# Optimization experiments

Hardware: AMD Instinct MI355X
Metric: run time of the kernel (lower is better)

Reference implementation:

```python
import jax, jax.numpy as jnp
import numpy as np

RADIUS = 0.2
NSAMPLE = 32
BANDWIDTH = 0.1


def ellipsoid_query(xyz, new_xyz, radius, nsample):
    """xyz:(B,N,3), new_xyz:(B,P,3) -> idx:(B,P,nsample) int32.
    Ellipsoid semi-axes (radius, 2*radius, radius); first nsample hits,
    padded with the first hit (index 0 if empty), matching the CUDA kernel.
    """
    B, N, _ = xyz.shape
    inv_sq = jnp.asarray([1.0 / radius**2, 1.0 / (2.0 * radius) ** 2, 1.0 / radius**2],
                         dtype=xyz.dtype)
    # accumulate per-coordinate to avoid a (B,P,N,3) intermediate
    q = jnp.zeros((B, new_xyz.shape[1], N), dtype=xyz.dtype)
    for k in range(3):
        d = new_xyz[:, :, None, k] - xyz[:, None, :, k]  # (B,P,N)
        q = q + d * d * inv_sq[k]
    mask = q < 1.0
    cand = jnp.where(mask, jnp.arange(N, dtype=jnp.int32), jnp.int32(N))  # invalid -> N
    cand = jnp.sort(cand, axis=-1)[..., :nsample]                          # (B,P,S)
    first = cand[..., :1]
    first = jnp.where(first >= N, jnp.int32(0), first)
    return jnp.where(cand >= N, first, cand)


def group(features, idx):
    """features:(B,C,N), idx:(B,P,S) -> (B,C,P,S)"""
    return jnp.take_along_axis(features[:, :, None, :], idx[:, None, :, :], axis=-1)


def setup_inputs() -> dict:
    key = jax.random.key(0)
    k1, k2, k3 = jax.random.split(key, 3)
    xyz = jax.random.uniform(k1, (4, 8192, 3), dtype=jnp.float32)
    new_xyz = jax.random.uniform(k2, (4, 2048, 3), dtype=jnp.float32)
    features = jax.random.normal(k3, (4, 64, 8192), dtype=jnp.float32)
    return {"xyz": xyz, "new_xyz": new_xyz, "features": features}


def reference(xyz, new_xyz, features):
    idx = ellipsoid_query(xyz, new_xyz, RADIUS, NSAMPLE)          # (B,P,S)
    xyz_trans = jnp.transpose(xyz, (0, 2, 1))                      # (B,3,N)
    grouped_xyz = group(xyz_trans, idx)                            # (B,3,P,S)
    # density: gaussian of distance to center
    g = jnp.transpose(grouped_xyz, (0, 2, 3, 1))                   # (B,P,S,3)
    dist = jnp.linalg.norm(g - new_xyz[:, :, None, :], axis=-1)    # (B,P,S)
    density = jnp.exp(-dist**2 / (2.0 * BANDWIDTH**2)) / (2.5 * BANDWIDTH)
    grouped_density = (1.0 / density)[:, None, :, :]               # (B,1,P,S)
    grouped_features = group(features, idx)                        # (B,C,P,S)
    return jnp.concatenate([grouped_xyz, grouped_density, grouped_features], axis=1)
```

## Files before the change

### kernel.cpp

```cpp
#include <hip/hip_runtime.h>

constexpr int NPTS = 8192;
constexpr int NQ   = 2048;
constexpr int NC   = 64;
constexpr int NS   = 32;
constexpr int NCH  = 3 + 1 + NC;
constexpr int CS   = NQ * NS;


__global__ __launch_bounds__(256, 8) void prep_kernel(
    const float* __restrict__ feat,
    const float* __restrict__ xyz,
    float* __restrict__ ftr,
    float* __restrict__ soa)
{
    const int b  = blockIdx.y;
    const int bx = blockIdx.x;
    const int t  = threadIdx.x;

    if (bx < NPTS / 64) {
        __shared__ float tile[NC][65];
        const int n0 = bx * 64;
        const float* fb = feat + (size_t)b * NC * NPTS;
        {
            const int pl = t & 63;
            const int c0 = t >> 6;
            #pragma unroll
            for (int i = 0; i < 16; ++i) {
                const int c = c0 + 4 * i;
                tile[c][pl] = fb[(size_t)c * NPTS + n0 + pl];
            }
        }
        __syncthreads();
        float* tb = ftr + ((size_t)b * NPTS + n0) * NC;
        {
            const int cl = t & 63;
            const int pb = t >> 6;
            #pragma unroll
            for (int i = 0; i < 16; ++i) {
                const int pp = pb + 4 * i;
                tb[(size_t)pp * NC + cl] = tile[cl][pp];
            }
        }
    } else {
        const int n0 = (bx - NPTS / 64) * 4096;
        const float* xb = xyz + (size_t)b * NPTS * 3;
        float* xs = soa + (size_t)b * 3 * NPTS;
        float* ys = xs + NPTS;
        float* zs = ys + NPTS;
        #pragma unroll
        for (int k = 0; k < 16; ++k) {
            const int i = n0 + k * 256 + t;
            xs[i] = xb[i * 3 + 0];
            ys[i] = xb[i * 3 + 1];
            zs[i] = xb[i * 3 + 2];
        }
    }
}

__global__ __launch_bounds__(256, 8) void scan_kernel(
    const float* __restrict__ soa,
    const float* __restrict__ nxyz,
    int* __restrict__ gidx,
    float* __restrict__ out)
{
    __shared__ int idx_s[4][NS];

    const int b    = blockIdx.y;
    const int tid  = threadIdx.x;
    const int lane = tid & 63;
    const int wave = tid >> 6;
    const int p    = blockIdx.x * 4 + wave;

    const float* xs = soa + (size_t)b * 3 * NPTS;
    const float* ys = xs + NPTS;
    const float* zs = ys + NPTS;
    int* idx_row = idx_s[wave];

    const float qx = nxyz[((size_t)b * NQ + p) * 3 + 0];
    const float qy = nxyz[((size_t)b * NQ + p) * 3 + 1];
    const float qz = nxyz[((size_t)b * NQ + p) * 3 + 2];

    int cnt = 0;
    int first = -1;

    float x0 = xs[lane],      y0 = ys[lane],      z0 = zs[lane];
    float x1 = xs[64 + lane], y1 = ys[64 + lane], z1 = zs[64 + lane];

    for (int base = 0; base < NPTS; base += 64) {
        float xn = 0.f, yn = 0.f, zn = 0.f;
        const int pf = base + 128;
        if (pf < NPTS) {
            xn = xs[pf + lane]; yn = ys[pf + lane]; zn = zs[pf + lane];
        }

        const float dx = __fsub_rn(qx, x0);
        const float dy = __fsub_rn(qy, y0);
        const float dz = __fsub_rn(qz, z0);
        const float t0 = __fmul_rn(__fmul_rn(dx, dx), 25.0f);
        const float t1 = __fmul_rn(__fmul_rn(dy, dy), 6.25f);
        const float t2 = __fmul_rn(__fmul_rn(dz, dz), 25.0f);
        const float qv = __fadd_rn(__fadd_rn(t0, t1), t2);
        const bool hit = qv < 1.0f;

        const unsigned long long m = __ballot(hit);
        if (first < 0 && m != 0ull)
            first = base + __builtin_ctzll(m);
        if (hit) {
            const int pos = cnt + __popcll(m & ((1ull << lane) - 1ull));
            if (pos < NS) idx_row[pos] = base + lane;
        }
        cnt += __popcll(m);
        if (cnt >= NS) break;

        x0 = x1; y0 = y1; z0 = z1;
        x1 = xn; y1 = yn; z1 = zn;
    }
    if (cnt < NS) {
        const int f = (cnt == 0) ? 0 : first;
        if (lane < NS && lane >= cnt) idx_row[lane] = f;
    }

    if (lane < NS) {
        const int s = lane;
        const int j = idx_row[s];
        gidx[((size_t)b * NQ + p) * NS + s] = j;

        const float px = xs[j], py = ys[j], pz = zs[j];
        const float dx = __fsub_rn(px, qx);
        const float dy = __fsub_rn(py, qy);
        const float dz = __fsub_rn(pz, qz);
        const float d2 = __fadd_rn(__fadd_rn(__fmul_rn(dx, dx), __fmul_rn(dy, dy)),
                                   __fmul_rn(dz, dz));
        const float dist = __fsqrt_rn(d2);
        const float arg  = __fdiv_rn(-__fmul_rn(dist, dist), 0.02f);
        const float density = __fmul_rn(expf(arg), 4.0f);
        const float gd = __fdiv_rn(1.0f, density);

        float* ob = out + ((size_t)b * NCH * NQ + p) * NS + s;
        ob[0 * (size_t)CS] = px;
        ob[1 * (size_t)CS] = py;
        ob[2 * (size_t)CS] = pz;
        ob[3 * (size_t)CS] = gd;
    }
}

__global__ __launch_bounds__(512, 8) void group_kernel(
    const int* __restrict__ gidx,
    const float* __restrict__ ftr,
    float* __restrict__ out)
{
    const int b   = blockIdx.y;
    const int tid = threadIdx.x;
    const int q   = tid >> 6;
    const int r   = tid & 63;
    const int s   = r & 31;
    const int p   = blockIdx.x * 8 + q;

    const int j = gidx[((size_t)b * NQ + p) * NS + s];

    float* ob = out + ((size_t)b * NCH * NQ + p) * NS + s;
    const float4* fp = (const float4*)(ftr + ((size_t)b * NPTS + j) * NC);
    const int cg0 = r >> 5;
    #pragma unroll
    for (int k = 0; k < 8; ++k) {
        const int cg = cg0 + 2 * k;
        const float4 v = fp[cg];
        float* oc = ob + (size_t)(4 + 4 * cg) * CS;
        oc[0 * (size_t)CS] = v.x;
        oc[1 * (size_t)CS] = v.y;
        oc[2 * (size_t)CS] = v.z;
        oc[3 * (size_t)CS] = v.w;
    }
}

__global__ __launch_bounds__(512, 8) void ellip_direct_kernel(
    const float* __restrict__ xyz,
    const float* __restrict__ nxyz,
    const float* __restrict__ feat,
    float* __restrict__ out)
{
    __shared__ int idx_s[8][NS];

    const int b    = blockIdx.y;
    const int p0   = blockIdx.x * 8;
    const int tid  = threadIdx.x;
    const int lane = tid & 63;
    const int wave = tid >> 6;
    const float* xb = xyz + (size_t)b * NPTS * 3;

    {
        const int p = p0 + wave;
        const float qx = nxyz[((size_t)b * NQ + p) * 3 + 0];
        const float qy = nxyz[((size_t)b * NQ + p) * 3 + 1];
        const float qz = nxyz[((size_t)b * NQ + p) * 3 + 2];
        int cnt = 0, first = -1;
        for (int base = 0; base < NPTS; base += 64) {
            const int i = base + lane;
            const float dx = __fsub_rn(qx, xb[i * 3 + 0]);
            const float dy = __fsub_rn(qy, xb[i * 3 + 1]);
            const float dz = __fsub_rn(qz, xb[i * 3 + 2]);
            const float t0 = __fmul_rn(__fmul_rn(dx, dx), 25.0f);
            const float t1 = __fmul_rn(__fmul_rn(dy, dy), 6.25f);
            const float t2 = __fmul_rn(__fmul_rn(dz, dz), 25.0f);
            const float qv = __fadd_rn(__fadd_rn(t0, t1), t2);
            const bool hit = qv < 1.0f;
            const unsigned long long m = __ballot(hit);
            if (first < 0 && m != 0ull) first = base + __builtin_ctzll(m);
            if (hit) {
                const int pos = cnt + __popcll(m & ((1ull << lane) - 1ull));
                if (pos < NS) idx_s[wave][pos] = i;
            }
            cnt += __popcll(m);
            if (cnt >= NS) break;
        }
        if (cnt < NS) {
            const int f = (cnt == 0) ? 0 : first;
            if (lane < NS && lane >= cnt) idx_s[wave][lane] = f;
        }
    }
    __syncthreads();

    const int s = tid & 31;
    const int h = (tid >> 5) & 1;
    const int q = tid >> 6;
    const int p = p0 + q;
    const int j = idx_s[q][s];
    float* ob = out + ((size_t)b * NCH * NQ + p) * NS + s;

    if (h == 0) {
        const float qx = nxyz[((size_t)b * NQ + p) * 3 + 0];
        const float qy = nxyz[((size_t)b * NQ + p) * 3 + 1];
        const float qz = nxyz[((size_t)b * NQ + p) * 3 + 2];
        const float px = xb[j * 3 + 0], py = xb[j * 3 + 1], pz = xb[j * 3 + 2];
        const float dx = __fsub_rn(px, qx);
        const float dy = __fsub_rn(py, qy);
        const float dz = __fsub_rn(pz, qz);
        const float d2 = __fadd_rn(__fadd_rn(__fmul_rn(dx, dx), __fmul_rn(dy, dy)),
                                   __fmul_rn(dz, dz));
        const float dist = __fsqrt_rn(d2);
        const float arg  = __fdiv_rn(-__fmul_rn(dist, dist), 0.02f);
        const float gd = __fdiv_rn(1.0f, __fmul_rn(expf(arg), 4.0f));
        ob[0 * (size_t)CS] = px;
        ob[1 * (size_t)CS] = py;
        ob[2 * (size_t)CS] = pz;
        ob[3 * (size_t)CS] = gd;
    }
    const float* fb = feat + (size_t)b * NC * NPTS + j;
    #pragma unroll 4
    for (int c = h; c < NC; c += 2)
        ob[(size_t)(4 + c) * CS] = fb[(size_t)c * NPTS];
}

extern "C" void kernel_launch(void* const* d_in, const int* in_sizes, int n_in,
                              void* d_out, int out_size, void* d_ws, size_t ws_size,
                              hipStream_t stream) {
    const float* xyz  = (const float*)d_in[0];
    const float* nxyz = (const float*)d_in[1];
    const float* feat = (const float*)d_in[2];
    float* out = (float*)d_out;

    const int B = in_sizes[0] / (NPTS * 3);
    const size_t ftr_f = (size_t)B * NPTS * NC;
    const size_t soa_f = (size_t)B * 3 * NPTS;
    const size_t idx_f = (size_t)B * NQ * NS;
    const size_t need  = (ftr_f + soa_f + idx_f) * 4;

    if (ws_size >= need) {
        float* ftr = (float*)d_ws;
        float* soa = ftr + ftr_f;
        int*   idx = (int*)(soa + soa_f);

        prep_kernel<<<dim3(NPTS / 64 + 2, B), 256, 0, stream>>>(feat, xyz, ftr, soa);
        scan_kernel<<<dim3(NQ / 4, B), 256, 0, stream>>>(soa, nxyz, idx, out);
        group_kernel<<<dim3(NQ / 8, B), 512, 0, stream>>>(idx, ftr, out);
    } else {
        ellip_direct_kernel<<<dim3(NQ / 8, B), 512, 0, stream>>>(xyz, nxyz, feat, out);
    }
}
```

Measured before the change: 113.4 us.

## Transpose gathered features through LDS for float4 output stores, one query per block

The group kernel now handles a single query point per block. It gathers 32 neighbour rows of 64 channels as float4 into a padded shared-memory tile, then writes the output as contiguous float4 stores per channel instead of scattered scalar stores. The 1D grid is remapped so that neighbouring blocks interleave across batches, which is meant to spread memory traffic. The cost is a shared-memory transpose, a barrier, and eight times more, smaller blocks.

```diff
diff --git a/kernel.cpp b/kernel.cpp
--- a/kernel.cpp
+++ b/kernel.cpp
@@ -148,30 +148,41 @@
 __global__ __launch_bounds__(512, 8) void group_kernel(
     const int* __restrict__ gidx,
     const float* __restrict__ ftr,
-    float* __restrict__ out)
-{
-    const int b   = blockIdx.y;
+    float* __restrict__ out,
+    int B)
+{
+    __shared__ float ldsc[NC][33];
+
+    const int g = blockIdx.x;
+    int b, p;
+    if (B == 4) {
+        b = (g & 7) >> 1;
+        p = ((g >> 3) << 1) | (g & 1);
+    } else {
+        b = g / NQ;
+        p = g - b * NQ;
+    }
     const int tid = threadIdx.x;
-    const int q   = tid >> 6;
-    const int r   = tid & 63;
-    const int s   = r & 31;
-    const int p   = blockIdx.x * 8 + q;
-
-    const int j = gidx[((size_t)b * NQ + p) * NS + s];
-
-    float* ob = out + ((size_t)b * NCH * NQ + p) * NS + s;
-    const float4* fp = (const float4*)(ftr + ((size_t)b * NPTS + j) * NC);
-    const int cg0 = r >> 5;
-    #pragma unroll
-    for (int k = 0; k < 8; ++k) {
-        const int cg = cg0 + 2 * k;
-        const float4 v = fp[cg];
-        float* oc = ob + (size_t)(4 + 4 * cg) * CS;
-        oc[0 * (size_t)CS] = v.x;
-        oc[1 * (size_t)CS] = v.y;
-        oc[2 * (size_t)CS] = v.z;
-        oc[3 * (size_t)CS] = v.w;
-    }
+
+    const int cg = tid & 15;
+    const int sl = tid >> 4;
+    const int j  = gidx[((size_t)b * NQ + p) * NS + sl];
+    const float4 v = ((const float4*)(ftr + ((size_t)b * NPTS + j) * NC))[cg];
+    ldsc[4 * cg + 0][sl] = v.x;
+    ldsc[4 * cg + 1][sl] = v.y;
+    ldsc[4 * cg + 2][sl] = v.z;
+    ldsc[4 * cg + 3][sl] = v.w;
+    __syncthreads();
+
+    const int c  = tid >> 3;
+    const int s4 = (tid & 7) << 2;
+    float4 w;
+    w.x = ldsc[c][s4 + 0];
+    w.y = ldsc[c][s4 + 1];
+    w.z = ldsc[c][s4 + 2];
+    w.w = ldsc[c][s4 + 3];
+    float* op = out + (((size_t)b * NCH + 4 + c) * NQ + p) * NS + s4;
+    *(float4*)op = w;
 }
 
 __global__ __launch_bounds__(512, 8) void ellip_direct_kernel(
@@ -273,7 +284,7 @@
 
         prep_kernel<<<dim3(NPTS / 64 + 2, B), 256, 0, stream>>>(feat, xyz, ftr, soa);
         scan_kernel<<<dim3(NQ / 4, B), 256, 0, stream>>>(soa, nxyz, idx, out);
-        group_kernel<<<dim3(NQ / 8, B), 512, 0, stream>>>(idx, ftr, out);
+        group_kernel<<<dim3(B * NQ), 512, 0, stream>>>(idx, ftr, out, B);
     } else {
         ellip_direct_kernel<<<dim3(NQ / 8, B), 512, 0, stream>>>(xyz, nxyz, feat, out);
     }
```

Measured after the change: 112.2 us. Within noise of the previous version (-1.0%).
